# Kernel tuning notes

Hardware: AMD Instinct MI355X
Metric: run time of the kernel (lower is better)

## Reference

```python
import jax, jax.numpy as jnp
import numpy as np

IN_H, IN_W = 512, 512
OUT_H, OUT_W = 512, 512
K = 8
BATCH = 64


def setup_inputs() -> dict:
    key = jax.random.key(0)
    k1, k2, k3 = jax.random.split(key, 3)
    inp = jax.random.normal(k1, (BATCH, IN_H, IN_W), dtype=jnp.float32)
    connections = jax.random.randint(k2, (OUT_H * OUT_W, K), 0, IN_H * IN_W, dtype=jnp.int32)
    bound = 1.0 / np.sqrt(K)
    weights = jax.random.uniform(k3, (OUT_H * OUT_W, K), dtype=jnp.float32, minval=-bound, maxval=bound)
    return {"input": inp, "connections": connections, "weights": weights}


def reference(input, connections, weights):
    # input: (B, H_in, W_in); connections/weights: (O, K) with O = OUT_H*OUT_W
    b = input.shape[0]
    x_flat = input.reshape(b, -1)                       # (B, N_in)
    gathered = jnp.take(x_flat, connections, axis=1)    # (B, O, K)
    out = jnp.einsum('bok,ok->bo', gathered, weights)   # (B, O)
    return out.reshape(b, OUT_H, OUT_W)
```

## Files before the change

### kernel.cpp

```cpp
#include <hip/hip_runtime.h>


#define IN_N  (512*512)
#define OUT_N (512*512)
#define BATCH 64
#define KCONN 8
#define TIDX  128

typedef float f32x4 __attribute__((ext_vector_type(4)));

__device__ inline unsigned short f2bf(float f) {
    unsigned u; __builtin_memcpy(&u, &f, 4);
    u = (u + 0x7fffu + ((u >> 16) & 1u)) >> 16;
    return (unsigned short)u;
}
__device__ inline float bflo(unsigned u) {
    unsigned v = u << 16; float f; __builtin_memcpy(&f, &v, 4); return f;
}
__device__ inline float bfhi(unsigned u) {
    unsigned v = u & 0xffff0000u; float f; __builtin_memcpy(&f, &v, 4); return f;
}

__global__ __launch_bounds__(256, 8) void transpose_kernel(const float* __restrict__ in,
                                                           unsigned short* __restrict__ xt) {
    __shared__ unsigned lds_u[BATCH][TIDX / 2 + 1];
    const int t    = threadIdx.x;
    const int idx0 = blockIdx.x * TIDX;

    const int lb = t >> 5;
    const int lc = (t & 31) << 2;
#pragma unroll
    for (int p = 0; p < 8; ++p) {
        const int b = p * 8 + lb;
        f32x4 v = __builtin_nontemporal_load(
            (const f32x4*)(in + (size_t)b * IN_N + idx0 + lc));
        const unsigned u0 = (unsigned)f2bf(v.x) | ((unsigned)f2bf(v.y) << 16);
        const unsigned u1 = (unsigned)f2bf(v.z) | ((unsigned)f2bf(v.w) << 16);
        lds_u[b][(lc >> 1) + 0] = u0;
        lds_u[b][(lc >> 1) + 1] = u1;
    }
    __syncthreads();

    const int si = t >> 3;
    const int sb = (t & 7) << 3;
#pragma unroll
    for (int p = 0; p < 2; ++p) {
        const int col = p * 32 + si;
        unsigned lo[4], hi[4];
#pragma unroll
        for (int j = 0; j < 4; ++j) {
            const unsigned a  = lds_u[sb + 2 * j + 0][col];
            const unsigned b2 = lds_u[sb + 2 * j + 1][col];
            lo[j] = (a & 0xffffu) | (b2 << 16);
            hi[j] = (a >> 16) | (b2 & 0xffff0000u);
        }
        union { unsigned u[4]; uint4 v; } pk;
        pk.u[0] = lo[0]; pk.u[1] = lo[1]; pk.u[2] = lo[2]; pk.u[3] = lo[3];
        *(uint4*)(xt + (size_t)(idx0 + 2 * col + 0) * BATCH + sb) = pk.v;
        pk.u[0] = hi[0]; pk.u[1] = hi[1]; pk.u[2] = hi[2]; pk.u[3] = hi[3];
        *(uint4*)(xt + (size_t)(idx0 + 2 * col + 1) * BATCH + sb) = pk.v;
    }
}

__global__ __launch_bounds__(256, 8) void gather_kernel(const unsigned short* __restrict__ xt,
                                                        const int* __restrict__ conn,
                                                        const float* __restrict__ w,
                                                        float* __restrict__ out) {
    const int t  = threadIdx.x;
    const int o0 = blockIdx.x * 32;
    const int ol = t >> 3;
    const int ch = t & 7;
    const int o  = o0 + ol;

    const int4   c0 = ((const int4*)conn)[(size_t)o * 2 + 0];
    const int4   c1 = ((const int4*)conn)[(size_t)o * 2 + 1];
    const float4 w0 = ((const float4*)w)[(size_t)o * 2 + 0];
    const float4 w1 = ((const float4*)w)[(size_t)o * 2 + 1];
    const int   cidx[KCONN] = {c0.x, c0.y, c0.z, c0.w, c1.x, c1.y, c1.z, c1.w};
    const float wk[KCONN]   = {w0.x, w0.y, w0.z, w0.w, w1.x, w1.y, w1.z, w1.w};

    float acc[8] = {0.f, 0.f, 0.f, 0.f, 0.f, 0.f, 0.f, 0.f};

#pragma unroll
    for (int k = 0; k < KCONN; ++k) {
        const uint4 r = *(const uint4*)(xt + (size_t)cidx[k] * BATCH + ch * 8);
        const unsigned q[4] = {r.x, r.y, r.z, r.w};
        const float wv = wk[k];
#pragma unroll
        for (int e = 0; e < 4; ++e) {
            acc[2 * e + 0] += bflo(q[e]) * wv;
            acc[2 * e + 1] += bfhi(q[e]) * wv;
        }
    }

#pragma unroll
    for (int j = 0; j < 8; ++j) {
        __builtin_nontemporal_store(acc[j], out + (size_t)(ch * 8 + j) * OUT_N + o);
    }
}

__global__ __launch_bounds__(256) void direct_kernel(const float* __restrict__ in,
                                                     const int* __restrict__ conn,
                                                     const float* __restrict__ w,
                                                     float* __restrict__ out) {
    const int o = blockIdx.x * 256 + threadIdx.x;

    const int4   c0 = ((const int4*)conn)[(size_t)o * 2 + 0];
    const int4   c1 = ((const int4*)conn)[(size_t)o * 2 + 1];
    const float4 w0 = ((const float4*)w)[(size_t)o * 2 + 0];
    const float4 w1 = ((const float4*)w)[(size_t)o * 2 + 1];

    const int   cidx[KCONN] = {c0.x, c0.y, c0.z, c0.w, c1.x, c1.y, c1.z, c1.w};
    const float wk[KCONN]   = {w0.x, w0.y, w0.z, w0.w, w1.x, w1.y, w1.z, w1.w};

    for (int b = 0; b < BATCH; ++b) {
        const float* xb = in + (size_t)b * IN_N;
        float acc = 0.0f;
#pragma unroll
        for (int k = 0; k < KCONN; ++k) acc += xb[cidx[k]] * wk[k];
        out[(size_t)b * OUT_N + o] = acc;
    }
}

extern "C" void kernel_launch(void* const* d_in, const int* in_sizes, int n_in,
                              void* d_out, int out_size, void* d_ws, size_t ws_size,
                              hipStream_t stream) {
    const float* inp  = (const float*)d_in[0];
    const int*   conn = (const int*)d_in[1];
    const float* w    = (const float*)d_in[2];
    float*       out  = (float*)d_out;

    const size_t xt_bytes = (size_t)IN_N * BATCH * sizeof(unsigned short);

    if (ws_size >= xt_bytes) {
        unsigned short* xt = (unsigned short*)d_ws;
        transpose_kernel<<<IN_N / TIDX, 256, 0, stream>>>(inp, xt);
        gather_kernel<<<OUT_N / 32, 256, 0, stream>>>(xt, conn, w, out);
    } else {
        direct_kernel<<<OUT_N / 256, 256, 0, stream>>>(inp, conn, w, out);
    }
}
```

Measured before the change: 193.9 us.

## Fuse transpose and gather into one cooperative persistent kernel with grid sync

Merges the bf16 transpose pass and the gather pass into a single persistent cooperative kernel. Blocks loop over transpose tiles, synchronise the whole grid, then loop over output tiles. This removes one kernel launch and the gap between the two kernels. The cost is a grid-wide barrier and a grid limited to occupancy, which may reduce latency hiding for the random gathers. It also rewrites the LDS unpack to build 16-bit elements one at a time and drops the nontemporal hint on output stores.

```diff
diff --git a/kernel.cpp b/kernel.cpp
--- a/kernel.cpp
+++ b/kernel.cpp
@@ -1,4 +1,7 @@
 #include <hip/hip_runtime.h>
+#include <hip/hip_cooperative_groups.h>
+
+namespace cg = cooperative_groups;
 
 
 #define IN_N  (512*512)
@@ -6,13 +9,14 @@
 #define BATCH 64
 #define KCONN 8
 #define TIDX  128
+#define NTILE (IN_N / TIDX)
+#define NOT   (OUT_N / 32)
 
 typedef float f32x4 __attribute__((ext_vector_type(4)));
 
-__device__ inline unsigned short f2bf(float f) {
+__device__ inline unsigned f2bf(float f) {
     unsigned u; __builtin_memcpy(&u, &f, 4);
-    u = (u + 0x7fffu + ((u >> 16) & 1u)) >> 16;
-    return (unsigned short)u;
+    return (u + 0x7fffu + ((u >> 16) & 1u)) >> 16;
 }
 __device__ inline float bflo(unsigned u) {
     unsigned v = u << 16; float f; __builtin_memcpy(&f, &v, 4); return f;
@@ -21,81 +25,77 @@
     unsigned v = u & 0xffff0000u; float f; __builtin_memcpy(&f, &v, 4); return f;
 }
 
-__global__ __launch_bounds__(256, 8) void transpose_kernel(const float* __restrict__ in,
-                                                           unsigned short* __restrict__ xt) {
+__global__ __launch_bounds__(256, 8) void fused_kernel(const float* __restrict__ in,
+                                                       unsigned short* __restrict__ xt,
+                                                       const int* __restrict__ conn,
+                                                       const float* __restrict__ w,
+                                                       float* __restrict__ out) {
     __shared__ unsigned lds_u[BATCH][TIDX / 2 + 1];
-    const int t    = threadIdx.x;
-    const int idx0 = blockIdx.x * TIDX;
+    const int t = threadIdx.x;
 
-    const int lb = t >> 5;
-    const int lc = (t & 31) << 2;
+    for (int tile = blockIdx.x; tile < NTILE; tile += gridDim.x) {
+        const int idx0 = tile * TIDX;
+        const int lb = t >> 5;
+        const int lc = (t & 31) << 2;
 #pragma unroll
-    for (int p = 0; p < 8; ++p) {
-        const int b = p * 8 + lb;
-        f32x4 v = __builtin_nontemporal_load(
-            (const f32x4*)(in + (size_t)b * IN_N + idx0 + lc));
-        const unsigned u0 = (unsigned)f2bf(v.x) | ((unsigned)f2bf(v.y) << 16);
-        const unsigned u1 = (unsigned)f2bf(v.z) | ((unsigned)f2bf(v.w) << 16);
-        lds_u[b][(lc >> 1) + 0] = u0;
-        lds_u[b][(lc >> 1) + 1] = u1;
+        for (int p = 0; p < 8; ++p) {
+            const int b = p * 8 + lb;
+            f32x4 v = __builtin_nontemporal_load(
+                (const f32x4*)(in + (size_t)b * IN_N + idx0 + lc));
+            lds_u[b][(lc >> 1) + 0] = f2bf(v.x) | (f2bf(v.y) << 16);
+            lds_u[b][(lc >> 1) + 1] = f2bf(v.z) | (f2bf(v.w) << 16);
+        }
+        __syncthreads();
+
+        const int rl = t >> 3;
+        const int sb = (t & 7) << 3;
+#pragma unroll
+        for (int p = 0; p < 4; ++p) {
+            const int i = p * 32 + rl;
+            const int c = i >> 1;
+            const int h = i & 1;
+            union { unsigned short s[8]; uint4 v4; } pk;
+#pragma unroll
+            for (int e = 0; e < 8; ++e) {
+                const unsigned u = lds_u[sb + e][c];
+                pk.s[e] = (unsigned short)(h ? (u >> 16) : (u & 0xffffu));
+            }
+            *(uint4*)(xt + (size_t)(idx0 + i) * BATCH + sb) = pk.v4;
+        }
+        __syncthreads();
     }
-    __syncthreads();
 
-    const int si = t >> 3;
-    const int sb = (t & 7) << 3;
-#pragma unroll
-    for (int p = 0; p < 2; ++p) {
-        const int col = p * 32 + si;
-        unsigned lo[4], hi[4];
-#pragma unroll
-        for (int j = 0; j < 4; ++j) {
-            const unsigned a  = lds_u[sb + 2 * j + 0][col];
-            const unsigned b2 = lds_u[sb + 2 * j + 1][col];
-            lo[j] = (a & 0xffffu) | (b2 << 16);
-            hi[j] = (a >> 16) | (b2 & 0xffff0000u);
-        }
-        union { unsigned u[4]; uint4 v; } pk;
-        pk.u[0] = lo[0]; pk.u[1] = lo[1]; pk.u[2] = lo[2]; pk.u[3] = lo[3];
-        *(uint4*)(xt + (size_t)(idx0 + 2 * col + 0) * BATCH + sb) = pk.v;
-        pk.u[0] = hi[0]; pk.u[1] = hi[1]; pk.u[2] = hi[2]; pk.u[3] = hi[3];
-        *(uint4*)(xt + (size_t)(idx0 + 2 * col + 1) * BATCH + sb) = pk.v;
-    }
-}
+    __threadfence();
+    cg::this_grid().sync();
 
-__global__ __launch_bounds__(256, 8) void gather_kernel(const unsigned short* __restrict__ xt,
-                                                        const int* __restrict__ conn,
-                                                        const float* __restrict__ w,
-                                                        float* __restrict__ out) {
-    const int t  = threadIdx.x;
-    const int o0 = blockIdx.x * 32;
     const int ol = t >> 3;
     const int ch = t & 7;
-    const int o  = o0 + ol;
+    for (int tile = blockIdx.x; tile < NOT; tile += gridDim.x) {
+        const int o = tile * 32 + ol;
 
-    const int4   c0 = ((const int4*)conn)[(size_t)o * 2 + 0];
-    const int4   c1 = ((const int4*)conn)[(size_t)o * 2 + 1];
-    const float4 w0 = ((const float4*)w)[(size_t)o * 2 + 0];
-    const float4 w1 = ((const float4*)w)[(size_t)o * 2 + 1];
-    const int   cidx[KCONN] = {c0.x, c0.y, c0.z, c0.w, c1.x, c1.y, c1.z, c1.w};
-    const float wk[KCONN]   = {w0.x, w0.y, w0.z, w0.w, w1.x, w1.y, w1.z, w1.w};
+        const int4   c0 = ((const int4*)conn)[(size_t)o * 2 + 0];
+        const int4   c1 = ((const int4*)conn)[(size_t)o * 2 + 1];
+        const float4 w0 = ((const float4*)w)[(size_t)o * 2 + 0];
+        const float4 w1 = ((const float4*)w)[(size_t)o * 2 + 1];
+        const int   cidx[KCONN] = {c0.x, c0.y, c0.z, c0.w, c1.x, c1.y, c1.z, c1.w};
+        const float wk[KCONN]   = {w0.x, w0.y, w0.z, w0.w, w1.x, w1.y, w1.z, w1.w};
 
-    float acc[8] = {0.f, 0.f, 0.f, 0.f, 0.f, 0.f, 0.f, 0.f};
-
+        float acc[8] = {0.f, 0.f, 0.f, 0.f, 0.f, 0.f, 0.f, 0.f};
 #pragma unroll
-    for (int k = 0; k < KCONN; ++k) {
-        const uint4 r = *(const uint4*)(xt + (size_t)cidx[k] * BATCH + ch * 8);
-        const unsigned q[4] = {r.x, r.y, r.z, r.w};
-        const float wv = wk[k];
+        for (int k = 0; k < KCONN; ++k) {
+            const uint4 r = *(const uint4*)(xt + (size_t)cidx[k] * BATCH + ch * 8);
+            const unsigned q[4] = {r.x, r.y, r.z, r.w};
+            const float wv = wk[k];
 #pragma unroll
-        for (int e = 0; e < 4; ++e) {
-            acc[2 * e + 0] += bflo(q[e]) * wv;
-            acc[2 * e + 1] += bfhi(q[e]) * wv;
+            for (int e = 0; e < 4; ++e) {
+                acc[2 * e + 0] += bflo(q[e]) * wv;
+                acc[2 * e + 1] += bfhi(q[e]) * wv;
+            }
         }
-    }
-
 #pragma unroll
-    for (int j = 0; j < 8; ++j) {
-        __builtin_nontemporal_store(acc[j], out + (size_t)(ch * 8 + j) * OUT_N + o);
+        for (int j = 0; j < 8; ++j) {
+            out[(size_t)(ch * 8 + j) * OUT_N + o] = acc[j];
+        }
     }
 }
 
@@ -132,10 +132,26 @@
 
     const size_t xt_bytes = (size_t)IN_N * BATCH * sizeof(unsigned short);
 
-    if (ws_size >= xt_bytes) {
+    static int coop_grid = -2;
+    if (coop_grid == -2) {
+        int blocksPerCU = 0, numCU = 0;
+        hipError_t e1 = hipOccupancyMaxActiveBlocksPerMultiprocessor(
+            &blocksPerCU, (const void*)fused_kernel, 256, 0);
+        hipError_t e2 = hipDeviceGetAttribute(
+            &numCU, hipDeviceAttributeMultiprocessorCount, 0);
+        if (e1 == hipSuccess && e2 == hipSuccess && blocksPerCU > 0 && numCU > 0) {
+            int g = blocksPerCU * numCU;
+            coop_grid = g < NTILE ? g : NTILE;
+        } else {
+            coop_grid = -1;
+        }
+    }
+
+    if (ws_size >= xt_bytes && coop_grid > 0) {
         unsigned short* xt = (unsigned short*)d_ws;
-        transpose_kernel<<<IN_N / TIDX, 256, 0, stream>>>(inp, xt);
-        gather_kernel<<<OUT_N / 32, 256, 0, stream>>>(xt, conn, w, out);
+        void* args[] = {(void*)&inp, (void*)&xt, (void*)&conn, (void*)&w, (void*)&out};
+        hipLaunchCooperativeKernel((const void*)fused_kernel,
+                                   dim3(coop_grid), dim3(256), args, 0, stream);
     } else {
         direct_kernel<<<OUT_N / 256, 256, 0, stream>>>(inp, conn, w, out);
     }
```

After: 374.8 us. 93.3% more time.
